# Kernel tuning notes

Measured on AMD Instinct MI355X. Metric: run time of the kernel, lower is better.

## Reference

```python
import jax, jax.numpy as jnp
import numpy as np

HEADS = 8
PATCH = 4  # stride == patch_size -> non-overlapping windows, no padding


def _make_pos_index(p: int) -> np.ndarray:
    coord = np.arange(p)
    coords = np.stack(np.meshgrid(coord, coord, indexing='ij'))  # [2,p,p]
    cf = coords.reshape(2, -1)  # [2,p^2]
    rel = cf[:, :, None] - cf[:, None, :]  # [2,p^2,p^2]
    rel = rel.transpose(1, 2, 0)
    rel[:, :, 0] += p - 1
    rel[:, :, 1] += p - 1
    rel[:, :, 0] *= 2 * p - 1
    return rel.sum(-1).astype(np.int32)  # [p^2,p^2]


def setup_inputs() -> dict:
    key = jax.random.key(0)
    k1, k2, k3, k4, k5 = jax.random.split(key, 5)
    b, dim, h = 8, 256, 160
    x = jax.random.normal(k1, (b, dim, h, h), dtype=jnp.float32)
    qkv_w = jax.random.normal(k2, (3 * dim,), dtype=jnp.float32)
    qkv_b = jax.random.normal(k3, (3 * dim,), dtype=jnp.float32) * 0.1
    pos_encode = jax.random.normal(k4, ((2 * PATCH - 1) ** 2, HEADS), dtype=jnp.float32) * 0.02
    out_w = jax.random.normal(k5, (dim, dim), dtype=jnp.float32) / np.sqrt(dim)
    pos_index = jnp.asarray(_make_pos_index(PATCH))
    return {"x": x, "qkv_w": qkv_w, "qkv_b": qkv_b, "pos_encode": pos_encode,
            "out_w": out_w, "pos_index": pos_index}


def reference(x, qkv_w, qkv_b, pos_encode, out_w, pos_index):
    b, dim, h, w = x.shape
    p = PATCH
    heads = HEADS
    hd = dim // heads
    Hp, Wp = h // p, w // p
    n = Hp * Wp  # patch_num
    scale = hd ** (-0.5)

    # depthwise 1x1 conv on cat([x,x,x]) == per-channel scale + bias
    qkv = jnp.concatenate([x, x, x], axis=1) * qkv_w[None, :, None, None] \
          + qkv_b[None, :, None, None]  # [b,3*dim,h,w]

    # window partition matching F.unfold ordering: channels-major, kernel row-major
    t = qkv.reshape(b, 3, heads, hd, Hp, p, Wp, p)
    # -> (3, b, heads, Hp, Wp, ph, pw, hd)
    t = t.transpose(1, 0, 2, 4, 6, 5, 7, 3).reshape(3, b, heads, n, p * p, hd)
    q, k, v = t[0], t[1], t[2]

    attn = jnp.einsum('bhnid,bhnjd->bhnij', q * scale, k)  # [b,heads,n,p^2,p^2]
    bias = pos_encode[pos_index]            # [p^2,p^2,heads]
    bias = bias.transpose(2, 0, 1)          # [heads,p^2,p^2]
    attn = jax.nn.softmax(attn + bias[None, :, None, :, :], axis=-1)
    out = jnp.einsum('bhnij,bhnjd->bhnid', attn, v)  # [b,heads,n,p^2,hd]

    # fold back (stride == patch -> exact inverse of partition)
    out = out.reshape(b, heads, Hp, Wp, p, p, hd)
    out = out.transpose(0, 1, 6, 2, 4, 3, 5).reshape(b, dim, h, w)

    # 1x1 conv, no bias
    return jnp.einsum('oc,bchw->bohw', out_w, out)
```

## Files before the change

kernel.cpp:

```cpp
#include <hip/hip_runtime.h>
#include <hip/hip_bf16.h>

#define B_    8
#define DIM   256
#define HH    160
#define WW_   160
#define NHEAD 8
#define HD    32
#define P_    4
#define WP_   40
#define NPW   1600
#define PP    16

#define NROWS 204800
#define HSTRIDE 6553600L

typedef __attribute__((ext_vector_type(8))) short bf16x8;
typedef __attribute__((ext_vector_type(4))) float f32x4;

__device__ __forceinline__ unsigned short f2b(float f) {
    __hip_bfloat16 h = __float2bfloat16(f);
    return *(unsigned short*)&h;
}

__global__ void convert_w_kernel(const float* __restrict__ w,
                                 short* __restrict__ wb)
{
    const int i = blockIdx.x * 256 + threadIdx.x;
    float4 v = ((const float4*)w)[i];
    short4 o;
    o.x = (short)f2b(v.x); o.y = (short)f2b(v.y);
    o.z = (short)f2b(v.z); o.w = (short)f2b(v.w);
    ((short4*)wb)[i] = o;
}

__launch_bounds__(128, 2)
__global__ void attn_kernel(const float* __restrict__ x,
                            const float* __restrict__ qkv_w,
                            const float* __restrict__ qkv_b,
                            const float* __restrict__ pos_encode,
                            const int* __restrict__ pos_index,
                            short* __restrict__ att)
{
    __shared__ float xs[4096];
    __shared__ float wqs[32], bqs[32], wks[32], bks[32], wvs[32], bvs[32];
    __shared__ float bias[256];

    const int t   = threadIdx.x;
    const int blk = blockIdx.x;
    const int wg  = blk % 5;
    int tmp = blk / 5;
    const int head = tmp & 7; tmp >>= 3;
    const int hp = tmp % 40;
    const int b  = tmp / 40;
    const int c0 = head * 32;
    const int h0 = hp * 4;
    const int w0 = wg * 32;

    if (t < 32) {
        wqs[t] = qkv_w[c0 + t];       bqs[t] = qkv_b[c0 + t];
        wks[t] = qkv_w[256 + c0 + t]; bks[t] = qkv_b[256 + c0 + t];
        wvs[t] = qkv_w[512 + c0 + t]; bvs[t] = qkv_b[512 + c0 + t];
    }
    bias[t]       = pos_encode[pos_index[t] * 8 + head];
    bias[t + 128] = pos_encode[pos_index[t + 128] * 8 + head];

    #pragma unroll
    for (int it = 0; it < 8; ++it) {
        const int idx  = t + it * 128;
        const int c    = idx >> 5;
        const int r    = (idx >> 3) & 3;
        const int col4 = idx & 7;
        const float4 v = *(const float4*)(x +
            (((long)(b * 256 + c0 + c) * 160) + h0 + r) * 160 + w0 + col4 * 4);
        *(float4*)&xs[idx * 4] = v;
    }
    __syncthreads();

    const int win = t >> 4, i = t & 15;
    const int iph = i >> 2, ipw = i & 3;
    const float scale = 0.17677669529663687f;

    float qk[32]; float qbk = 0.f;
    {
        const int qb = iph * 32 + win * 4 + ipw;
        #pragma unroll
        for (int d = 0; d < 32; ++d) {
            const float q = (xs[d * 128 + qb] * wqs[d] + bqs[d]) * scale;
            qk[d] = q * wks[d];
            qbk  += q * bks[d];
        }
    }

    float s[16];
    #pragma unroll
    for (int j = 0; j < 16; ++j) {
        const int jb = (j >> 2) * 32 + win * 4 + (j & 3);
        float acc = qbk;
        #pragma unroll
        for (int d = 0; d < 32; ++d) acc += qk[d] * xs[d * 128 + jb];
        s[j] = acc + bias[i * 16 + j];
    }

    float m = s[0];
    #pragma unroll
    for (int j = 1; j < 16; ++j) m = fmaxf(m, s[j]);
    float l = 0.f;
    #pragma unroll
    for (int j = 0; j < 16; ++j) { s[j] = __expf(s[j] - m); l += s[j]; }
    const float inv = 1.f / l;

    unsigned int ow[16];
    #pragma unroll
    for (int d2 = 0; d2 < 16; ++d2) {
        const int d0 = d2 * 2;
        float a0 = 0.f, a1 = 0.f;
        #pragma unroll
        for (int j = 0; j < 16; ++j) {
            const int jb = (j >> 2) * 32 + win * 4 + (j & 3);
            a0 += s[j] * xs[d0 * 128 + jb];
            a1 += s[j] * xs[d0 * 128 + 128 + jb];
        }
        a0 = a0 * inv * wvs[d0]     + bvs[d0];
        a1 = a1 * inv * wvs[d0 + 1] + bvs[d0 + 1];
        ow[d2] = (unsigned int)f2b(a0) | ((unsigned int)f2b(a1) << 16);
    }

    const int  R    = ((b * 40 + hp) * 4 + iph) * 160 + w0 + win * 4 + ipw;
    short* dst = att + (long)head * HSTRIDE + (long)R * 32;
    uint4 v0 = {ow[0],  ow[1],  ow[2],  ow[3]};
    uint4 v1 = {ow[4],  ow[5],  ow[6],  ow[7]};
    uint4 v2 = {ow[8],  ow[9],  ow[10], ow[11]};
    uint4 v3 = {ow[12], ow[13], ow[14], ow[15]};
    *(uint4*)(dst +  0) = v0;
    *(uint4*)(dst +  8) = v1;
    *(uint4*)(dst + 16) = v2;
    *(uint4*)(dst + 24) = v3;
}

__launch_bounds__(256, 2)
__global__ void conv_kernel(const short* __restrict__ att,
                            const short* __restrict__ wb,
                            float* __restrict__ y)
{
    const int blk = blockIdx.x;
    const int sl = blk & 7;
    const int og = (blk >> 3) & 3;
    const int sh = blk >> 5;
    const int s  = sh * 8 + sl;
    const int b  = s / 40;
    const int hp = s % 40;

    const int t    = threadIdx.x;
    const int ph   = t >> 6;
    const int lane = t & 63;
    const int m16  = lane & 15;
    const int kq   = lane >> 4;

    bf16x8 wfr[4][8];
    #pragma unroll
    for (int nt = 0; nt < 4; ++nt)
        #pragma unroll
        for (int kk = 0; kk < 8; ++kk)
            wfr[nt][kk] = *(const bf16x8*)(wb +
                ((og * 64 + nt * 16 + m16) * 256 + kk * 32 + kq * 8));

    const int  R0   = s * 640 + ph * 160;
    const short* arow = att + (long)(R0 + m16) * 32 + kq * 8;
    float* yo = y + ((long)(b * 256 + og * 64) * 160 + (hp * 4 + ph)) * 160;

    const f32x4 zf = {0.f, 0.f, 0.f, 0.f};
    bf16x8 bA[8], bB[8];

#define LB(dstb, cc_) { \
    _Pragma("unroll") \
    for (int kk = 0; kk < 8; ++kk) \
        dstb[kk] = *(const bf16x8*)(arow + kk * HSTRIDE + (cc_) * 512); }

#define COMP(bfb, cc_) { \
    f32x4 a0 = zf, a1 = zf, a2 = zf, a3 = zf; \
    _Pragma("unroll") \
    for (int kk = 0; kk < 8; ++kk) { \
        a0 = __builtin_amdgcn_mfma_f32_16x16x32_bf16(wfr[0][kk], bfb[kk], a0, 0, 0, 0); \
        a1 = __builtin_amdgcn_mfma_f32_16x16x32_bf16(wfr[1][kk], bfb[kk], a1, 0, 0, 0); \
        a2 = __builtin_amdgcn_mfma_f32_16x16x32_bf16(wfr[2][kk], bfb[kk], a2, 0, 0, 0); \
        a3 = __builtin_amdgcn_mfma_f32_16x16x32_bf16(wfr[3][kk], bfb[kk], a3, 0, 0, 0); \
    } \
    _Pragma("unroll") \
    for (int r = 0; r < 4; ++r) { \
        const int oo = kq * 4 + r; \
        yo[(long)(oo     ) * 25600 + (cc_) * 16 + m16] = a0[r]; \
        yo[(long)(oo + 16) * 25600 + (cc_) * 16 + m16] = a1[r]; \
        yo[(long)(oo + 32) * 25600 + (cc_) * 16 + m16] = a2[r]; \
        yo[(long)(oo + 48) * 25600 + (cc_) * 16 + m16] = a3[r]; \
    } }

    LB(bA, 0);
    #pragma unroll
    for (int c2 = 0; c2 < 5; ++c2) {
        LB(bB, 2 * c2 + 1);
        COMP(bA, 2 * c2);
        if (c2 < 4) LB(bA, 2 * c2 + 2);
        COMP(bB, 2 * c2 + 1);
    }
#undef LB
#undef COMP
}

__launch_bounds__(256, 2)
__global__ void patchsa_fused(const float* __restrict__ x,
                              const float* __restrict__ qkv_w,
                              const float* __restrict__ qkv_b,
                              const float* __restrict__ pos_encode,
                              const short* __restrict__ w_bf16,
                              const int* __restrict__ pos_index,
                              float* __restrict__ y)
{
    __shared__ float wql[768];
    __shared__ float bql[768];
    __shared__ float pel[392];
    __shared__ int   pil[256];
    __shared__ float q4[NHEAD * 528];
    __shared__ float k4[NHEAD * 528];
    __shared__ float v4[NHEAD * 528];
    __shared__ float probs[2048];
    __shared__ alignas(16) short att3[4096];

    const int t   = threadIdx.x;
    const int blk = blockIdx.x;
    const int b   = blk / NPW;
    const int n   = blk % NPW;
    const int hp  = n / WP_;
    const int wp  = n % WP_;
    const int h0  = hp * P_;
    const int w0  = wp * P_;

    for (int idx = t; idx < 768; idx += 256) {
        wql[idx] = qkv_w[idx];
        bql[idx] = qkv_b[idx];
    }
    for (int idx = t; idx < 392; idx += 256)
        pel[idx] = pos_encode[idx];
    pil[t] = pos_index[t];
    __syncthreads();

    for (int task = t; task < 1024; task += 256) {
        const int c  = task & 255;
        const int ph = task >> 8;
        const float* xr = x + ((((long)b * DIM + c) * HH) + h0 + ph) * WW_ + w0;
        float4 xv = *(const float4*)xr;
        const int head = c >> 5, d = c & 31;
        const float wq = wql[c],      bq = bql[c];
        const float wk = wql[256+c],  bk = bql[256+c];
        const float wv = wql[512+c],  bv = bql[512+c];
        const int base = head * 528 + d;
        const int p0 = ph * 4;
        float xf[4] = {xv.x, xv.y, xv.z, xv.w};
        #pragma unroll
        for (int pw = 0; pw < 4; ++pw) {
            const int off = base + (p0 + pw) * 33;
            q4[off] = xf[pw] * wq + bq;
            k4[off] = xf[pw] * wk + bk;
            v4[off] = xf[pw] * wv + bv;
        }
    }
    __syncthreads();

    if (t < 128) {
        const int head = t >> 4, i = t & 15;
        const float scale = 0.17677669529663687f;
        float qr[32];
        const int qb = head * 528 + i * 33;
        #pragma unroll
        for (int d = 0; d < 32; ++d) qr[d] = q4[qb + d];
        float s[16];
        #pragma unroll
        for (int j = 0; j < 16; ++j) {
            const int kb = head * 528 + j * 33;
            float acc = 0.f;
            #pragma unroll
            for (int d = 0; d < 32; ++d) acc += qr[d] * k4[kb + d];
            s[j] = acc * scale + pel[pil[i * 16 + j] * NHEAD + head];
        }
        float m = s[0];
        #pragma unroll
        for (int j = 1; j < 16; ++j) m = fmaxf(m, s[j]);
        float l = 0.f;
        #pragma unroll
        for (int j = 0; j < 16; ++j) { s[j] = __expf(s[j] - m); l += s[j]; }
        const float inv = 1.f / l;
        #pragma unroll
        for (int j = 0; j < 16; ++j)
            probs[(head * 16 + i) * 16 + j] = s[j] * inv;
    }
    __syncthreads();

    {
        const int head = t >> 5, d = t & 31;
        float vr[16];
        const int vb = head * 528 + d;
        #pragma unroll
        for (int j = 0; j < 16; ++j) vr[j] = v4[vb + j * 33];
        const int k = t;
        const int abase = (k >> 3) * 128 + (k & 7);
        #pragma unroll
        for (int i = 0; i < 16; ++i) {
            const float* pr = &probs[(head * 16 + i) * 16];
            float acc = 0.f;
            #pragma unroll
            for (int j = 0; j < 16; ++j) acc += pr[j] * vr[j];
            att3[abase + i * 8] = (short)f2b(acc);
        }
    }
    __syncthreads();

    {
        const int wave = t >> 6, lane = t & 63;
        const int m16  = lane & 15, kq = lane >> 4;
        const int nbase = wave * 64;
        f32x4 acc0 = {0.f, 0.f, 0.f, 0.f};
        f32x4 acc1 = acc0, acc2 = acc0, acc3 = acc0;
        #pragma unroll
        for (int kk = 0; kk < 8; ++kk) {
            const int k0 = kk * 32 + kq * 8;
            bf16x8 a = *(const bf16x8*)&att3[(k0 >> 3) * 128 + m16 * 8];
            bf16x8 b0 = *(const bf16x8*)&w_bf16[(nbase +  0 + m16) * 256 + k0];
            bf16x8 b1 = *(const bf16x8*)&w_bf16[(nbase + 16 + m16) * 256 + k0];
            bf16x8 b2 = *(const bf16x8*)&w_bf16[(nbase + 32 + m16) * 256 + k0];
            bf16x8 b3 = *(const bf16x8*)&w_bf16[(nbase + 48 + m16) * 256 + k0];
            acc0 = __builtin_amdgcn_mfma_f32_16x16x32_bf16(a, b0, acc0, 0, 0, 0);
            acc1 = __builtin_amdgcn_mfma_f32_16x16x32_bf16(a, b1, acc1, 0, 0, 0);
            acc2 = __builtin_amdgcn_mfma_f32_16x16x32_bf16(a, b2, acc2, 0, 0, 0);
            acc3 = __builtin_amdgcn_mfma_f32_16x16x32_bf16(a, b3, acc3, 0, 0, 0);
        }
        f32x4 accs[4] = {acc0, acc1, acc2, acc3};
        #pragma unroll
        for (int nt = 0; nt < 4; ++nt) {
            const int o = nbase + nt * 16 + m16;
            const long ob = (((long)b * DIM + o) * HH) * WW_;
            #pragma unroll
            for (int r = 0; r < 4; ++r) {
                const int pos = kq * 4 + r;
                const int ph = pos >> 2, pw = pos & 3;
                y[ob + (long)(h0 + ph) * WW_ + (w0 + pw)] = accs[nt][r];
            }
        }
    }
}

extern "C" void kernel_launch(void* const* d_in, const int* in_sizes, int n_in,
                              void* d_out, int out_size, void* d_ws, size_t ws_size,
                              hipStream_t stream) {
    const float* x          = (const float*)d_in[0];
    const float* qkv_w      = (const float*)d_in[1];
    const float* qkv_b      = (const float*)d_in[2];
    const float* pos_encode = (const float*)d_in[3];
    const float* out_w      = (const float*)d_in[4];
    const int*   pos_index  = (const int*)d_in[5];
    float* y = (float*)d_out;
    short* w_bf16 = (short*)d_ws;

    convert_w_kernel<<<dim3(64), dim3(256), 0, stream>>>(out_w, w_bf16);

    const size_t need = 131072 + (size_t)NROWS * 256 * 2;
    if (ws_size >= need) {
        short* att = w_bf16 + 65536;
        attn_kernel<<<dim3(12800), dim3(128), 0, stream>>>(
            x, qkv_w, qkv_b, pos_encode, pos_index, att);
        conv_kernel<<<dim3(1280), dim3(256), 0, stream>>>(att, w_bf16, y);
    } else {
        patchsa_fused<<<dim3(B_ * NPW), dim3(256), 0, stream>>>(
            x, qkv_w, qkv_b, pos_encode, w_bf16, pos_index, y);
    }
}
```

Baseline: 731.8 us.

## Swizzle LDS layouts, stage conv weights in LDS, coalesce attention output stores

The attention kernel now XOR-swizzles the x tile in shared memory, pads the bias table to avoid bank conflicts, and routes outputs through LDS so each row segment is written contiguously. The conv kernel loads its 64x256 bf16 weight slice into swizzled LDS once per block instead of holding 32 bf16x8 fragments in registers per thread, and both kernels raise their occupancy hints. The fallback fused kernel and the workspace-size check are removed. This is meant to cut register pressure and LDS conflicts and to improve store coalescing, at the cost of extra LDS reads per MFMA and an extra barrier.

```diff
diff --git a/kernel.cpp b/kernel.cpp
--- a/kernel.cpp
+++ b/kernel.cpp
@@ -34,7 +34,7 @@
     ((short4*)wb)[i] = o;
 }
 
-__launch_bounds__(128, 2)
+__launch_bounds__(128, 4)
 __global__ void attn_kernel(const float* __restrict__ x,
                             const float* __restrict__ qkv_w,
                             const float* __restrict__ qkv_b,
@@ -44,7 +44,7 @@
 {
     __shared__ float xs[4096];
     __shared__ float wqs[32], bqs[32], wks[32], bks[32], wvs[32], bvs[32];
-    __shared__ float bias[256];
+    __shared__ float bias[272];
 
     const int t   = threadIdx.x;
     const int blk = blockIdx.x;
@@ -62,8 +62,13 @@
         wks[t] = qkv_w[256 + c0 + t]; bks[t] = qkv_b[256 + c0 + t];
         wvs[t] = qkv_w[512 + c0 + t]; bvs[t] = qkv_b[512 + c0 + t];
     }
-    bias[t]       = pos_encode[pos_index[t] * 8 + head];
-    bias[t + 128] = pos_encode[pos_index[t + 128] * 8 + head];
+    {
+        const int i0 = t >> 4, j0 = t & 15;
+        bias[i0 * 17 + j0] = pos_encode[pos_index[t] * 8 + head];
+        const int t2 = t + 128;
+        const int i1 = t2 >> 4, j1 = t2 & 15;
+        bias[i1 * 17 + j1] = pos_encode[pos_index[t2] * 8 + head];
+    }
 
     #pragma unroll
     for (int it = 0; it < 8; ++it) {
@@ -73,7 +78,7 @@
         const int col4 = idx & 7;
         const float4 v = *(const float4*)(x +
             (((long)(b * 256 + c0 + c) * 160) + h0 + r) * 160 + w0 + col4 * 4);
-        *(float4*)&xs[idx * 4] = v;
+        *(float4*)&xs[c * 128 + r * 32 + ((col4 * 4) ^ (r * 8))] = v;
     }
     __syncthreads();
 
@@ -81,25 +86,24 @@
     const int iph = i >> 2, ipw = i & 3;
     const float scale = 0.17677669529663687f;
 
+    #define XADDR(d_, r_, col_) ((d_) * 128 + (r_) * 32 + ((col_) ^ ((r_) * 8)))
+
     float qk[32]; float qbk = 0.f;
-    {
-        const int qb = iph * 32 + win * 4 + ipw;
-        #pragma unroll
-        for (int d = 0; d < 32; ++d) {
-            const float q = (xs[d * 128 + qb] * wqs[d] + bqs[d]) * scale;
-            qk[d] = q * wks[d];
-            qbk  += q * bks[d];
-        }
+    #pragma unroll
+    for (int d = 0; d < 32; ++d) {
+        const float q = (xs[XADDR(d, iph, win * 4 + ipw)] * wqs[d] + bqs[d]) * scale;
+        qk[d] = q * wks[d];
+        qbk  += q * bks[d];
     }
 
     float s[16];
     #pragma unroll
     for (int j = 0; j < 16; ++j) {
-        const int jb = (j >> 2) * 32 + win * 4 + (j & 3);
+        const int jr = j >> 2, jc = win * 4 + (j & 3);
         float acc = qbk;
         #pragma unroll
-        for (int d = 0; d < 32; ++d) acc += qk[d] * xs[d * 128 + jb];
-        s[j] = acc + bias[i * 16 + j];
+        for (int d = 0; d < 32; ++d) acc += qk[d] * xs[XADDR(d, jr, jc)];
+        s[j] = acc + bias[i * 17 + j];
     }
 
     float m = s[0];
@@ -117,32 +121,49 @@
         float a0 = 0.f, a1 = 0.f;
         #pragma unroll
         for (int j = 0; j < 16; ++j) {
-            const int jb = (j >> 2) * 32 + win * 4 + (j & 3);
-            a0 += s[j] * xs[d0 * 128 + jb];
-            a1 += s[j] * xs[d0 * 128 + 128 + jb];
+            const int jr = j >> 2, jc = win * 4 + (j & 3);
+            a0 += s[j] * xs[XADDR(d0,     jr, jc)];
+            a1 += s[j] * xs[XADDR(d0 + 1, jr, jc)];
         }
         a0 = a0 * inv * wvs[d0]     + bvs[d0];
         a1 = a1 * inv * wvs[d0 + 1] + bvs[d0 + 1];
         ow[d2] = (unsigned int)f2b(a0) | ((unsigned int)f2b(a1) << 16);
     }
-
-    const int  R    = ((b * 40 + hp) * 4 + iph) * 160 + w0 + win * 4 + ipw;
-    short* dst = att + (long)head * HSTRIDE + (long)R * 32;
-    uint4 v0 = {ow[0],  ow[1],  ow[2],  ow[3]};
-    uint4 v1 = {ow[4],  ow[5],  ow[6],  ow[7]};
-    uint4 v2 = {ow[8],  ow[9],  ow[10], ow[11]};
-    uint4 v3 = {ow[12], ow[13], ow[14], ow[15]};
-    *(uint4*)(dst +  0) = v0;
-    *(uint4*)(dst +  8) = v1;
-    *(uint4*)(dst + 16) = v2;
-    *(uint4*)(dst + 24) = v3;
-}
-
-__launch_bounds__(256, 2)
+    #undef XADDR
+
+    __syncthreads();
+    unsigned int* Tu = (unsigned int*)xs;
+    {
+        const int tb = (iph * 32 + win * 4 + ipw) * 20;
+        uint4 v0 = {ow[0],  ow[1],  ow[2],  ow[3]};
+        uint4 v1 = {ow[4],  ow[5],  ow[6],  ow[7]};
+        uint4 v2 = {ow[8],  ow[9],  ow[10], ow[11]};
+        uint4 v3 = {ow[12], ow[13], ow[14], ow[15]};
+        *(uint4*)&Tu[tb +  0] = v0;
+        *(uint4*)&Tu[tb +  4] = v1;
+        *(uint4*)&Tu[tb +  8] = v2;
+        *(uint4*)&Tu[tb + 12] = v3;
+    }
+    __syncthreads();
+    {
+        short* dstB = att + (long)head * HSTRIDE
+                          + ((long)((b * 40 + hp) * 4) * 160 + w0) * 32;
+        #pragma unroll
+        for (int k2 = 0; k2 < 4; ++k2) {
+            const int rr = k2 * 32 + (t >> 2);
+            uint4 v = *(const uint4*)&Tu[rr * 20 + (t & 3) * 4];
+            *(uint4*)(dstB + (long)k2 * (160 * 32) + t * 8) = v;
+        }
+    }
+}
+
+__launch_bounds__(256, 4)
 __global__ void conv_kernel(const short* __restrict__ att,
                             const short* __restrict__ wb,
                             float* __restrict__ y)
 {
+    __shared__ short wlds[64 * 256];
+
     const int blk = blockIdx.x;
     const int sl = blk & 7;
     const int og = (blk >> 3) & 3;
@@ -157,13 +178,21 @@
     const int m16  = lane & 15;
     const int kq   = lane >> 4;
 
-    bf16x8 wfr[4][8];
-    #pragma unroll
-    for (int nt = 0; nt < 4; ++nt)
-        #pragma unroll
-        for (int kk = 0; kk < 8; ++kk)
-            wfr[nt][kk] = *(const bf16x8*)(wb +
-                ((og * 64 + nt * 16 + m16) * 256 + kk * 32 + kq * 8));
+    {
+        const char* wsrc = (const char*)(wb + og * 64 * 256);
+        #pragma unroll
+        for (int it = 0; it < 8; ++it) {
+            const int byteoff = (t + it * 256) * 16;
+            const int row = byteoff >> 9;
+            const int swz = byteoff ^ ((row & 7) << 4);
+            uint4 v = *(const uint4*)(wsrc + byteoff);
+            *(uint4*)((char*)wlds + swz) = v;
+        }
+    }
+    __syncthreads();
+
+    #define WF(nt_, kk_) (*(const bf16x8*)((const char*)wlds + \
+        ((((nt_) * 16 + m16) * 512 + (kk_) * 64 + kq * 16) ^ ((m16 & 7) << 4))))
 
     const int  R0   = s * 640 + ph * 160;
     const short* arow = att + (long)(R0 + m16) * 32 + kq * 8;
@@ -181,10 +210,11 @@
     f32x4 a0 = zf, a1 = zf, a2 = zf, a3 = zf; \
     _Pragma("unroll") \
     for (int kk = 0; kk < 8; ++kk) { \
-        a0 = __builtin_amdgcn_mfma_f32_16x16x32_bf16(wfr[0][kk], bfb[kk], a0, 0, 0, 0); \
-        a1 = __builtin_amdgcn_mfma_f32_16x16x32_bf16(wfr[1][kk], bfb[kk], a1, 0, 0, 0); \
-        a2 = __builtin_amdgcn_mfma_f32_16x16x32_bf16(wfr[2][kk], bfb[kk], a2, 0, 0, 0); \
-        a3 = __builtin_amdgcn_mfma_f32_16x16x32_bf16(wfr[3][kk], bfb[kk], a3, 0, 0, 0); \
+        bf16x8 w0 = WF(0, kk), w1 = WF(1, kk), w2 = WF(2, kk), w3 = WF(3, kk); \
+        a0 = __builtin_amdgcn_mfma_f32_16x16x32_bf16(w0, bfb[kk], a0, 0, 0, 0); \
+        a1 = __builtin_amdgcn_mfma_f32_16x16x32_bf16(w1, bfb[kk], a1, 0, 0, 0); \
+        a2 = __builtin_amdgcn_mfma_f32_16x16x32_bf16(w2, bfb[kk], a2, 0, 0, 0); \
+        a3 = __builtin_amdgcn_mfma_f32_16x16x32_bf16(w3, bfb[kk], a3, 0, 0, 0); \
     } \
     _Pragma("unroll") \
     for (int r = 0; r < 4; ++r) { \
@@ -205,147 +235,7 @@
     }
 #undef LB
 #undef COMP
-}
-
-__launch_bounds__(256, 2)
-__global__ void patchsa_fused(const float* __restrict__ x,
-                              const float* __restrict__ qkv_w,
-                              const float* __restrict__ qkv_b,
-                              const float* __restrict__ pos_encode,
-                              const short* __restrict__ w_bf16,
-                              const int* __restrict__ pos_index,
-                              float* __restrict__ y)
-{
-    __shared__ float wql[768];
-    __shared__ float bql[768];
-    __shared__ float pel[392];
-    __shared__ int   pil[256];
-    __shared__ float q4[NHEAD * 528];
-    __shared__ float k4[NHEAD * 528];
-    __shared__ float v4[NHEAD * 528];
-    __shared__ float probs[2048];
-    __shared__ alignas(16) short att3[4096];
-
-    const int t   = threadIdx.x;
-    const int blk = blockIdx.x;
-    const int b   = blk / NPW;
-    const int n   = blk % NPW;
-    const int hp  = n / WP_;
-    const int wp  = n % WP_;
-    const int h0  = hp * P_;
-    const int w0  = wp * P_;
-
-    for (int idx = t; idx < 768; idx += 256) {
-        wql[idx] = qkv_w[idx];
-        bql[idx] = qkv_b[idx];
-    }
-    for (int idx = t; idx < 392; idx += 256)
-        pel[idx] = pos_encode[idx];
-    pil[t] = pos_index[t];
-    __syncthreads();
-
-    for (int task = t; task < 1024; task += 256) {
-        const int c  = task & 255;
-        const int ph = task >> 8;
-        const float* xr = x + ((((long)b * DIM + c) * HH) + h0 + ph) * WW_ + w0;
-        float4 xv = *(const float4*)xr;
-        const int head = c >> 5, d = c & 31;
-        const float wq = wql[c],      bq = bql[c];
-        const float wk = wql[256+c],  bk = bql[256+c];
-        const float wv = wql[512+c],  bv = bql[512+c];
-        const int base = head * 528 + d;
-        const int p0 = ph * 4;
-        float xf[4] = {xv.x, xv.y, xv.z, xv.w};
-        #pragma unroll
-        for (int pw = 0; pw < 4; ++pw) {
-            const int off = base + (p0 + pw) * 33;
-            q4[off] = xf[pw] * wq + bq;
-            k4[off] = xf[pw] * wk + bk;
-            v4[off] = xf[pw] * wv + bv;
-        }
-    }
-    __syncthreads();
-
-    if (t < 128) {
-        const int head = t >> 4, i = t & 15;
-        const float scale = 0.17677669529663687f;
-        float qr[32];
-        const int qb = head * 528 + i * 33;
-        #pragma unroll
-        for (int d = 0; d < 32; ++d) qr[d] = q4[qb + d];
-        float s[16];
-        #pragma unroll
-        for (int j = 0; j < 16; ++j) {
-            const int kb = head * 528 + j * 33;
-            float acc = 0.f;
-            #pragma unroll
-            for (int d = 0; d < 32; ++d) acc += qr[d] * k4[kb + d];
-            s[j] = acc * scale + pel[pil[i * 16 + j] * NHEAD + head];
-        }
-        float m = s[0];
-        #pragma unroll
-        for (int j = 1; j < 16; ++j) m = fmaxf(m, s[j]);
-        float l = 0.f;
-        #pragma unroll
-        for (int j = 0; j < 16; ++j) { s[j] = __expf(s[j] - m); l += s[j]; }
-        const float inv = 1.f / l;
-        #pragma unroll
-        for (int j = 0; j < 16; ++j)
-            probs[(head * 16 + i) * 16 + j] = s[j] * inv;
-    }
-    __syncthreads();
-
-    {
-        const int head = t >> 5, d = t & 31;
-        float vr[16];
-        const int vb = head * 528 + d;
-        #pragma unroll
-        for (int j = 0; j < 16; ++j) vr[j] = v4[vb + j * 33];
-        const int k = t;
-        const int abase = (k >> 3) * 128 + (k & 7);
-        #pragma unroll
-        for (int i = 0; i < 16; ++i) {
-            const float* pr = &probs[(head * 16 + i) * 16];
-            float acc = 0.f;
-            #pragma unroll
-            for (int j = 0; j < 16; ++j) acc += pr[j] * vr[j];
-            att3[abase + i * 8] = (short)f2b(acc);
-        }
-    }
-    __syncthreads();
-
-    {
-        const int wave = t >> 6, lane = t & 63;
-        const int m16  = lane & 15, kq = lane >> 4;
-        const int nbase = wave * 64;
-        f32x4 acc0 = {0.f, 0.f, 0.f, 0.f};
-        f32x4 acc1 = acc0, acc2 = acc0, acc3 = acc0;
-        #pragma unroll
-        for (int kk = 0; kk < 8; ++kk) {
-            const int k0 = kk * 32 + kq * 8;
-            bf16x8 a = *(const bf16x8*)&att3[(k0 >> 3) * 128 + m16 * 8];
-            bf16x8 b0 = *(const bf16x8*)&w_bf16[(nbase +  0 + m16) * 256 + k0];
-            bf16x8 b1 = *(const bf16x8*)&w_bf16[(nbase + 16 + m16) * 256 + k0];
-            bf16x8 b2 = *(const bf16x8*)&w_bf16[(nbase + 32 + m16) * 256 + k0];
-            bf16x8 b3 = *(const bf16x8*)&w_bf16[(nbase + 48 + m16) * 256 + k0];
-            acc0 = __builtin_amdgcn_mfma_f32_16x16x32_bf16(a, b0, acc0, 0, 0, 0);
-            acc1 = __builtin_amdgcn_mfma_f32_16x16x32_bf16(a, b1, acc1, 0, 0, 0);
-            acc2 = __builtin_amdgcn_mfma_f32_16x16x32_bf16(a, b2, acc2, 0, 0, 0);
-            acc3 = __builtin_amdgcn_mfma_f32_16x16x32_bf16(a, b3, acc3, 0, 0, 0);
-        }
-        f32x4 accs[4] = {acc0, acc1, acc2, acc3};
-        #pragma unroll
-        for (int nt = 0; nt < 4; ++nt) {
-            const int o = nbase + nt * 16 + m16;
-            const long ob = (((long)b * DIM + o) * HH) * WW_;
-            #pragma unroll
-            for (int r = 0; r < 4; ++r) {
-                const int pos = kq * 4 + r;
-                const int ph = pos >> 2, pw = pos & 3;
-                y[ob + (long)(h0 + ph) * WW_ + (w0 + pw)] = accs[nt][r];
-            }
-        }
-    }
+#undef WF
 }
 
 extern "C" void kernel_launch(void* const* d_in, const int* in_sizes, int n_in,
@@ -359,17 +249,10 @@
     const int*   pos_index  = (const int*)d_in[5];
     float* y = (float*)d_out;
     short* w_bf16 = (short*)d_ws;
+    short* att = w_bf16 + 65536;
 
     convert_w_kernel<<<dim3(64), dim3(256), 0, stream>>>(out_w, w_bf16);
-
-    const size_t need = 131072 + (size_t)NROWS * 256 * 2;
-    if (ws_size >= need) {
-        short* att = w_bf16 + 65536;
-        attn_kernel<<<dim3(12800), dim3(128), 0, stream>>>(
-            x, qkv_w, qkv_b, pos_encode, pos_index, att);
-        conv_kernel<<<dim3(1280), dim3(256), 0, stream>>>(att, w_bf16, y);
-    } else {
-        patchsa_fused<<<dim3(B_ * NPW), dim3(256), 0, stream>>>(
-            x, qkv_w, qkv_b, pos_encode, w_bf16, pos_index, y);
-    }
-}
+    attn_kernel<<<dim3(12800), dim3(128), 0, stream>>>(
+        x, qkv_w, qkv_b, pos_encode, pos_index, att);
+    conv_kernel<<<dim3(1280), dim3(256), 0, stream>>>(att, w_bf16, y);
+}
```

Result: slower. 2.181 ms (+198.1%).
